# Optimization experiments

Hardware: AMD Instinct MI355X
Metric: run time of the kernel (lower is better)

The kernel has to match this reference:

```python
import jax, jax.numpy as jnp
import numpy as np

TEMP = 0.5  # init kwarg `tmp`
NUM_CLASSES = 100


def setup_inputs() -> dict:
    key = jax.random.key(0)
    k1, k2 = jax.random.split(key)
    embedding = jax.random.normal(k1, (8192, 256), dtype=jnp.float32)
    label = jax.random.randint(k2, (8192,), 0, NUM_CLASSES, dtype=jnp.int64)
    return {"embedding": embedding, "label": label}


def reference(embedding, label):
    # Row-normalize -> pairwise cosine similarity [N, N]
    normed = embedding / jnp.linalg.norm(embedding, axis=1, keepdims=True)
    sim = (normed @ normed.T) / TEMP  # already divided by temperature

    N = embedding.shape[0]
    eye = jnp.eye(N, dtype=bool)

    # Denominator: sum of exp(sim) over off-diagonal entries per row
    exp_sim = jnp.exp(sim)
    row_sum = jnp.sum(jnp.where(eye, 0.0, exp_sim), axis=1)  # [N]

    # log(exp(sim_ij) / row_sum_i) = sim_ij - log(row_sum_i)
    log_prob = sim - jnp.log(row_sum)[:, None]

    # Positive mask: same label, i != j
    pos_mask = (label[:, None] == label[None, :]) & ~eye
    n_i = jnp.sum(pos_mask, axis=1)  # positives per anchor

    inner = jnp.sum(jnp.where(pos_mask, log_prob, 0.0), axis=1)  # [N]
    per_anchor = jnp.where(n_i > 0, -inner / jnp.maximum(n_i, 1).astype(sim.dtype), 0.0)
    return jnp.sum(per_anchor)
```

## Files before the change

kernel.cpp:

```cpp
#include <hip/hip_runtime.h>
#include <hip/hip_bf16.h>
#include <stdint.h>

#define N    8192
#define D    256
#define NCLS 100

static constexpr float TEMP    = 0.5f;
static constexpr float SCALE_F = 1.69864360f;
static constexpr float E2      = 7.38905609893065f;
static constexpr float LN2     = 0.69314718055994531f;

typedef float f32x4 __attribute__((ext_vector_type(4)));

__device__ __forceinline__ unsigned short f2bf(float f) {
  union { float f; unsigned int u; } x; x.f = f;
  unsigned int r = x.u + 0x7fffu + ((x.u >> 16) & 1u);
  return (unsigned short)(r >> 16);
}
__device__ __forceinline__ float bf2f(unsigned short b) {
  union { unsigned int u; float f; } x; x.u = ((unsigned int)b) << 16;
  return x.f;
}
__device__ __forceinline__ void gld16(const void* g, void* l) {
  __builtin_amdgcn_global_load_lds(
      (const __attribute__((address_space(1))) unsigned int*)g,
      (__attribute__((address_space(3))) unsigned int*)l, 16, 0, 0);
}


__global__ __launch_bounds__(256) void normalize_kernel(
    const float* __restrict__ emb, const long long* __restrict__ label,
    unsigned short* __restrict__ abf, unsigned char* __restrict__ a8,
    float* __restrict__ rowsum, int* __restrict__ cnt,
    int* __restrict__ list) {
  const int row  = blockIdx.x * 4 + (threadIdx.x >> 6);
  const int lane = threadIdx.x & 63;
  const float4 v = ((const float4*)(emb + (size_t)row * D))[lane];
  float ss = v.x * v.x + v.y * v.y + v.z * v.z + v.w * v.w;
#pragma unroll
  for (int off = 1; off < 64; off <<= 1) ss += __shfl_xor(ss, off);
  const float s = rsqrtf(ss) * SCALE_F;
  const float x = v.x * s, y = v.y * s, z = v.z * s, wv = v.w * s;

  ushort4 o;
  o.x = f2bf(x); o.y = f2bf(y); o.z = f2bf(z); o.w = f2bf(wv);
  ((ushort4*)(abf + (size_t)row * D))[lane] = o;

  int p = __builtin_amdgcn_cvt_pk_fp8_f32(x, y, 0, false);
  p = __builtin_amdgcn_cvt_pk_fp8_f32(z, wv, p, true);
  *(int*)(a8 + (size_t)(row >> 4) * 4096 + (lane >> 1) * 128 +
          (row & 15) * 8 + (lane & 1) * 4) = p;

  if (lane == 0) {
    rowsum[row] = 0.f;
    const int c = (int)label[row];
    const int slot = atomicAdd(cnt + c, 1);
    list[c * 256 + slot] = row;
  }
}

#define TM 128
#define TN 128
#define JT 4

__global__ __launch_bounds__(256) void simexp_rowsum_kernel(
    const unsigned char* __restrict__ A, float* __restrict__ rowsum) {
  __shared__ __align__(16) unsigned char sa[TM * 256];
  __shared__ __align__(16) unsigned char sb[2][TN * 128];
  const int tid  = threadIdx.x;
  const int w    = tid >> 6;
  const int lane = tid & 63;
  const int quad = lane >> 4;
  const int l15  = lane & 15;
  const int row0 = blockIdx.y * TM;
  const int jc0  = blockIdx.x * (TN * JT);
  const int pr0  = row0 >> 4;
  const int pam  = (w & 1) * 4;
  const int pbn  = (w >> 1) * 4;
  const int wm   = (w & 1) * 64;

#pragma unroll
  for (int p = 0; p < 8; ++p) {
    const int seg = w * 8 + p;
    gld16(A + (size_t)(pr0 + (seg >> 2)) * 4096 + (seg & 3) * 1024 + lane * 16,
          sa + seg * 1024);
  }
#pragma unroll
  for (int p = 0; p < 4; ++p) {
    const int seg = w * 4 + p;
    gld16(A + (size_t)((jc0 >> 4) + (seg >> 1)) * 4096 + (seg & 1) * 1024 +
              lane * 16,
          sb[0] + seg * 1024);
  }
  __syncthreads();

  float rowpart[4][4];
#pragma unroll
  for (int mt = 0; mt < 4; ++mt)
#pragma unroll
    for (int e = 0; e < 4; ++e) rowpart[mt][e] = 0.f;

  int buf = 0;
  for (int jt = 0; jt < JT; ++jt) {
    f32x4 acc[4][4];
#pragma unroll
    for (int mt = 0; mt < 4; ++mt)
#pragma unroll
      for (int nt = 0; nt < 4; ++nt) acc[mt][nt] = (f32x4){0.f, 0.f, 0.f, 0.f};

#pragma unroll
    for (int kc = 0; kc < 2; ++kc) {
      if (!(jt == JT - 1 && kc == 1)) {
        const int njt = (kc == 1) ? jt + 1 : jt;
        const int nkc = kc ^ 1;
        const int pj0 = (jc0 + njt * TN) >> 4;
#pragma unroll
        for (int p = 0; p < 4; ++p) {
          const int seg = w * 4 + p;
          gld16(A + (size_t)(pj0 + (seg >> 1)) * 4096 + nkc * 2048 +
                    (seg & 1) * 1024 + lane * 16,
                sb[buf ^ 1] + seg * 1024);
        }
      }
#pragma unroll
      for (int kk = 0; kk < 4; ++kk) {
        const int fo = (kk * 4 + quad) * 128 + l15 * 8;
        long af[4], bf[4];
#pragma unroll
        for (int mt = 0; mt < 4; ++mt)
          af[mt] = *(const long*)(sa + (pam + mt) * 4096 + kc * 2048 + fo);
#pragma unroll
        for (int nt = 0; nt < 4; ++nt)
          bf[nt] = *(const long*)(sb[buf] + (pbn + nt) * 2048 + fo);
#pragma unroll
        for (int mt = 0; mt < 4; ++mt)
#pragma unroll
          for (int nt = 0; nt < 4; ++nt)
            acc[mt][nt] = __builtin_amdgcn_mfma_f32_16x16x32_fp8_fp8(
                af[mt], bf[nt], acc[mt][nt], 0, 0, 0);
      }
      __syncthreads();
      buf ^= 1;
    }

#pragma unroll
    for (int mt = 0; mt < 4; ++mt)
#pragma unroll
      for (int nt = 0; nt < 4; ++nt)
#pragma unroll
        for (int e = 0; e < 4; ++e)
          rowpart[mt][e] += __builtin_amdgcn_exp2f(acc[mt][nt][e]);
  }

#pragma unroll
  for (int mt = 0; mt < 4; ++mt)
#pragma unroll
    for (int e = 0; e < 4; ++e) {
      float v = rowpart[mt][e];
      v += __shfl_xor(v, 1);
      v += __shfl_xor(v, 2);
      v += __shfl_xor(v, 4);
      v += __shfl_xor(v, 8);
      if (l15 == 0)
        atomicAdd(&rowsum[row0 + wm + mt * 16 + quad * 4 + e], v);
    }
}

__global__ __launch_bounds__(256) void finalize_kernel(
    const unsigned short* __restrict__ abf, const float* __restrict__ rowsum,
    const long long* __restrict__ label, const int* __restrict__ cnt,
    const int* __restrict__ list, float* __restrict__ out) {
  __shared__ float red[4];
  __shared__ int rows_l[256];
  const int tid  = threadIdx.x;
  const int w    = tid >> 6;
  const int lane = tid & 63;

  if (blockIdx.x < NCLS) {
    const int c = blockIdx.x;
    const int m = cnt[c];
    if (m <= 1) return;
    if (tid < m) rows_l[tid] = list[c * 256 + tid];
    __syncthreads();
    float acc = 0.f;
    for (int s = 0; s < m; ++s)
      acc += bf2f(abf[(size_t)rows_l[s] * D + tid]);
    float v = acc * acc;
#pragma unroll
    for (int off = 1; off < 64; off <<= 1) v += __shfl_xor(v, off);
    if (lane == 0) red[w] = v;
    __syncthreads();
    if (tid == 0) {
      const float ssq = red[0] + red[1] + red[2] + red[3];
      const float term = (ssq * LN2 - 2.0f * (float)m) / (float)(m - 1);
      atomicAdd(out, -term);
    }
  } else {
    const int i = (blockIdx.x - NCLS) * 256 + tid;
    const int c = (int)label[i];
    float v = 0.f;
    if (cnt[c] > 1)
      v = __builtin_amdgcn_logf(rowsum[i] - E2) * LN2;
#pragma unroll
    for (int off = 1; off < 64; off <<= 1) v += __shfl_xor(v, off);
    if (lane == 0) red[w] = v;
    __syncthreads();
    if (tid == 0)
      atomicAdd(out, red[0] + red[1] + red[2] + red[3]);
  }
}

extern "C" void kernel_launch(void* const* d_in, const int* in_sizes, int n_in,
                              void* d_out, int out_size, void* d_ws,
                              size_t ws_size, hipStream_t stream) {
  const float* emb = (const float*)d_in[0];
  const long long* label = (const long long*)d_in[1];
  float* out = (float*)d_out;

  char* ws = (char*)d_ws;
  unsigned short* abf = (unsigned short*)ws;
  unsigned char* a8 = (unsigned char*)(ws + (size_t)N * D * 2);
  float* rowsum = (float*)(ws + (size_t)N * D * 3);
  int* cnt = (int*)(rowsum + N);
  int* list = cnt + 128;

  hipMemsetAsync(cnt, 0, 128 * 4, stream);
  hipMemsetAsync(out, 0, sizeof(float), stream);

  normalize_kernel<<<N / 4, 256, 0, stream>>>(emb, label, abf, a8, rowsum,
                                              cnt, list);

  dim3 gridB(N / (TN * JT), N / TM);
  simexp_rowsum_kernel<<<gridB, 256, 0, stream>>>(a8, rowsum);

  finalize_kernel<<<NCLS + N / 256, 256, 0, stream>>>(abf, rowsum, label, cnt,
                                                      list, out);
}
```

Baseline: 131.6 us.

## Exploit similarity symmetry: compute upper-triangular tiles and add column sums

The row-sum kernel now skips tiles entirely below the diagonal. Each computed tile's exp values are added both to its rows and, through a column reduction with extra atomics, to its columns. On diagonal tiles only strictly upper entries are kept, so the diagonal is excluded directly and the E2 subtraction in finalize goes away. The K-chunk for B shrinks to 64 bytes per stage, which halves B shared memory, and the launch bounds now ask for 3 blocks per CU. The aim is to roughly halve the MFMA and exp work, at the cost of more atomics and unbalanced work across blocks.

```diff
diff --git a/kernel.cpp b/kernel.cpp
--- a/kernel.cpp
+++ b/kernel.cpp
@@ -8,7 +8,6 @@
 
 static constexpr float TEMP    = 0.5f;
 static constexpr float SCALE_F = 1.69864360f;
-static constexpr float E2      = 7.38905609893065f;
 static constexpr float LN2     = 0.69314718055994531f;
 
 typedef float f32x4 __attribute__((ext_vector_type(4)));
@@ -64,10 +63,10 @@
 #define TN 128
 #define JT 4
 
-__global__ __launch_bounds__(256) void simexp_rowsum_kernel(
+__global__ __launch_bounds__(256, 3) void simexp_rowsum_kernel(
     const unsigned char* __restrict__ A, float* __restrict__ rowsum) {
   __shared__ __align__(16) unsigned char sa[TM * 256];
-  __shared__ __align__(16) unsigned char sb[2][TN * 128];
+  __shared__ __align__(16) unsigned char sb[2][TN * 64];
   const int tid  = threadIdx.x;
   const int w    = tid >> 6;
   const int lane = tid & 63;
@@ -75,10 +74,14 @@
   const int l15  = lane & 15;
   const int row0 = blockIdx.y * TM;
   const int jc0  = blockIdx.x * (TN * JT);
-  const int pr0  = row0 >> 4;
-  const int pam  = (w & 1) * 4;
-  const int pbn  = (w >> 1) * 4;
-  const int wm   = (w & 1) * 64;
+  if (row0 >= jc0 + TN * JT) return;
+  const int sdiag = (row0 >= jc0) ? ((row0 - jc0) >> 7) : -1;
+  const int jt0   = (sdiag >= 0) ? sdiag : 0;
+  const int pr0 = row0 >> 4;
+  const int pam = (w & 1) * 4;
+  const int pbn = (w >> 1) * 4;
+  const int wm  = (w & 1) * 64;
+  const int jn0 = (w >> 1) * 64;
 
 #pragma unroll
   for (int p = 0; p < 8; ++p) {
@@ -86,12 +89,13 @@
     gld16(A + (size_t)(pr0 + (seg >> 2)) * 4096 + (seg & 3) * 1024 + lane * 16,
           sa + seg * 1024);
   }
-#pragma unroll
-  for (int p = 0; p < 4; ++p) {
-    const int seg = w * 4 + p;
-    gld16(A + (size_t)((jc0 >> 4) + (seg >> 1)) * 4096 + (seg & 1) * 1024 +
-              lane * 16,
-          sb[0] + seg * 1024);
+  {
+    const int pj0 = (jc0 + jt0 * TN) >> 4;
+#pragma unroll
+    for (int p = 0; p < 2; ++p) {
+      const int seg = w * 2 + p;
+      gld16(A + (size_t)(pj0 + seg) * 4096 + lane * 16, sb[0] + seg * 1024);
+    }
   }
   __syncthreads();
 
@@ -102,7 +106,7 @@
     for (int e = 0; e < 4; ++e) rowpart[mt][e] = 0.f;
 
   int buf = 0;
-  for (int jt = 0; jt < JT; ++jt) {
+  for (int jt = jt0; jt < JT; ++jt) {
     f32x4 acc[4][4];
 #pragma unroll
     for (int mt = 0; mt < 4; ++mt)
@@ -110,29 +114,28 @@
       for (int nt = 0; nt < 4; ++nt) acc[mt][nt] = (f32x4){0.f, 0.f, 0.f, 0.f};
 
 #pragma unroll
-    for (int kc = 0; kc < 2; ++kc) {
-      if (!(jt == JT - 1 && kc == 1)) {
-        const int njt = (kc == 1) ? jt + 1 : jt;
-        const int nkc = kc ^ 1;
+    for (int kq = 0; kq < 4; ++kq) {
+      if (!(jt == JT - 1 && kq == 3)) {
+        const int njt = (kq == 3) ? jt + 1 : jt;
+        const int nkq = (kq + 1) & 3;
         const int pj0 = (jc0 + njt * TN) >> 4;
 #pragma unroll
-        for (int p = 0; p < 4; ++p) {
-          const int seg = w * 4 + p;
-          gld16(A + (size_t)(pj0 + (seg >> 1)) * 4096 + nkc * 2048 +
-                    (seg & 1) * 1024 + lane * 16,
+        for (int p = 0; p < 2; ++p) {
+          const int seg = w * 2 + p;
+          gld16(A + (size_t)(pj0 + seg) * 4096 + nkq * 1024 + lane * 16,
                 sb[buf ^ 1] + seg * 1024);
         }
       }
 #pragma unroll
-      for (int kk = 0; kk < 4; ++kk) {
-        const int fo = (kk * 4 + quad) * 128 + l15 * 8;
+      for (int kkl = 0; kkl < 2; ++kkl) {
+        const int fo = (kkl * 4 + quad) * 128 + l15 * 8;
         long af[4], bf[4];
 #pragma unroll
         for (int mt = 0; mt < 4; ++mt)
-          af[mt] = *(const long*)(sa + (pam + mt) * 4096 + kc * 2048 + fo);
+          af[mt] = *(const long*)(sa + (pam + mt) * 4096 + kq * 1024 + fo);
 #pragma unroll
         for (int nt = 0; nt < 4; ++nt)
-          bf[nt] = *(const long*)(sb[buf] + (pbn + nt) * 2048 + fo);
+          bf[nt] = *(const long*)(sb[buf] + (pbn + nt) * 1024 + fo);
 #pragma unroll
         for (int mt = 0; mt < 4; ++mt)
 #pragma unroll
@@ -144,13 +147,31 @@
       buf ^= 1;
     }
 
+    const bool diag = (jt == sdiag);
+    float colpart[4] = {0.f, 0.f, 0.f, 0.f};
 #pragma unroll
     for (int mt = 0; mt < 4; ++mt)
 #pragma unroll
       for (int nt = 0; nt < 4; ++nt)
 #pragma unroll
-        for (int e = 0; e < 4; ++e)
-          rowpart[mt][e] += __builtin_amdgcn_exp2f(acc[mt][nt][e]);
+        for (int e = 0; e < 4; ++e) {
+          float v = __builtin_amdgcn_exp2f(acc[mt][nt][e]);
+          if (diag) {
+            const int iloc = wm + mt * 16 + quad * 4 + e;
+            const int jloc = jn0 + nt * 16 + l15;
+            v = (iloc < jloc) ? v : 0.f;
+          }
+          rowpart[mt][e] += v;
+          colpart[nt] += v;
+        }
+#pragma unroll
+    for (int nt = 0; nt < 4; ++nt) {
+      float v = colpart[nt];
+      v += __shfl_xor(v, 16);
+      v += __shfl_xor(v, 32);
+      if (quad == 0)
+        atomicAdd(&rowsum[jc0 + jt * TN + jn0 + nt * 16 + l15], v);
+    }
   }
 
 #pragma unroll
@@ -201,7 +222,7 @@
     const int c = (int)label[i];
     float v = 0.f;
     if (cnt[c] > 1)
-      v = __builtin_amdgcn_logf(rowsum[i] - E2) * LN2;
+      v = __builtin_amdgcn_logf(rowsum[i]) * LN2;
 #pragma unroll
     for (int off = 1; off < 64; off <<= 1) v += __shfl_xor(v, off);
     if (lane == 0) red[w] = v;
```

Result: slower. 135.3 us (+2.9%).
